# Performance work log

Measured on AMD Instinct MI355X. Metric: run time of the kernel, lower is better.

Reference implementation:

```python
import jax, jax.numpy as jnp
import numpy as np

N_NODES = 100000
N_EDGES = 1600000
N_FEAT = 256
HIDDEN = 128
N_CLASSES = 40


def gcn_conv(x, edge_index, W, b, num_nodes):
    # h = X W  (transform first, like torch_geometric GCNConv)
    h = x @ W  # [N, out]
    # add self loops
    loops = jnp.arange(num_nodes, dtype=edge_index.dtype)
    src = jnp.concatenate([edge_index[0], loops])
    dst = jnp.concatenate([edge_index[1], loops])
    # symmetric normalization: deg computed on dst (in-degree incl. self loop)
    deg = jax.ops.segment_sum(jnp.ones_like(dst, dtype=h.dtype), dst,
                              num_segments=num_nodes)
    dinv = jnp.where(deg > 0, jax.lax.rsqrt(deg), 0.0)
    norm = dinv[src] * dinv[dst]  # [E+N]
    # gather -> scale -> scatter-add
    msgs = h[src] * norm[:, None]
    out = jax.ops.segment_sum(msgs, dst, num_segments=num_nodes)
    return out + b


def setup_inputs() -> dict:
    key = jax.random.key(0)
    k1, k2, k3, k4, k5 = jax.random.split(key, 5)
    x = jax.random.normal(k1, (N_NODES, N_FEAT), dtype=jnp.float32)
    edge_index = jax.random.randint(k2, (2, N_EDGES), 0, N_NODES, dtype=jnp.int64)
    W1 = jax.random.normal(k3, (N_FEAT, HIDDEN), dtype=jnp.float32) * (1.0 / np.sqrt(N_FEAT))
    b1 = jnp.zeros((HIDDEN,), dtype=jnp.float32)
    W2 = jax.random.normal(k4, (HIDDEN, N_CLASSES), dtype=jnp.float32) * (1.0 / np.sqrt(HIDDEN))
    b2 = jnp.zeros((N_CLASSES,), dtype=jnp.float32)
    return {"x": x, "edge_index": edge_index, "W1": W1, "b1": b1, "W2": W2, "b2": b2}


def reference(x, edge_index, W1, b1, W2, b2):
    num_nodes = x.shape[0]
    h = gcn_conv(x, edge_index, W1, b1, num_nodes)
    h = jax.nn.relu(h)
    # dropout p=0.1 is identity in eval mode (self.training == False)
    out = gcn_conv(h, edge_index, W2, b2, num_nodes)
    return out
```

## Files before the change

### kernel.cpp

```cpp
#include <hip/hip_runtime.h>


#define NFEAT 256
#define HID   128
#define NCLS  40
#define NBMAX 3136

__global__ __launch_bounds__(256) void kA_bhist(const int* __restrict__ dst,
                                                int* __restrict__ bcount, int E, int NB) {
    __shared__ int hist[NBMAX];
    for (int i = threadIdx.x; i < NB; i += 256) hist[i] = 0;
    __syncthreads();
    int stride = gridDim.x * blockDim.x;
    for (int e = blockIdx.x * blockDim.x + threadIdx.x; e < E; e += stride)
        atomicAdd(&hist[dst[e] >> 5], 1);
    __syncthreads();
    for (int i = threadIdx.x; i < NB; i += 256) {
        int h = hist[i];
        if (h) atomicAdd(&bcount[i], h);
    }
}

__global__ __launch_bounds__(256) void kB_bscan(const int* __restrict__ bcount,
                                                int* __restrict__ bstart,
                                                int* __restrict__ bcursor,
                                                int* __restrict__ rowptr,
                                                int NB, int Nn, int E) {
    __shared__ int sums[256];
    int t = threadIdx.x;
    int per = (NB + 255) / 256;
    int base = t * per;
    int s = 0;
    for (int j = 0; j < per; j++) {
        int i = base + j;
        if (i < NB) s += bcount[i];
    }
    sums[t] = s;
    __syncthreads();
    for (int off = 1; off < 256; off <<= 1) {
        int v = (t >= off) ? sums[t - off] : 0;
        __syncthreads();
        sums[t] += v;
        __syncthreads();
    }
    int run = sums[t] - s;
    for (int j = 0; j < per; j++) {
        int i = base + j;
        if (i < NB) { bstart[i] = run; bcursor[i] = run; run += bcount[i]; }
    }
    if (t == 255) { bstart[NB] = run; rowptr[Nn] = E; }
}

__global__ __launch_bounds__(256) void kC_scatter(const int* __restrict__ src,
                                                  const int* __restrict__ dst,
                                                  int* __restrict__ bcursor,
                                                  unsigned int* __restrict__ stage, int E) {
    int stride = gridDim.x * blockDim.x;
    for (int e = blockIdx.x * blockDim.x + threadIdx.x; e < E; e += stride) {
        int d = dst[e];
        int pos = atomicAdd(&bcursor[d >> 5], 1);
        stage[pos] = (unsigned int)src[e] | ((unsigned int)(d & 31) << 27);
    }
}

__global__ __launch_bounds__(256) void kD_fill(const unsigned int* __restrict__ stage,
                                               const int* __restrict__ bstart,
                                               int* __restrict__ rowptr,
                                               float* __restrict__ dinv,
                                               int* __restrict__ col, int Nn) {
    __shared__ int deg32[32];
    __shared__ int pref[32];
    __shared__ int cur[32];
    int b = blockIdx.x;
    int t = threadIdx.x;
    int bs = bstart[b], be = bstart[b + 1];
    if (t < 32) deg32[t] = 0;
    __syncthreads();
    for (int i = bs + t; i < be; i += 256) {
        unsigned int u = stage[i];
        atomicAdd(&deg32[u >> 27], 1);
    }
    __syncthreads();
    if (t == 0) {
        int r = 0;
        for (int j = 0; j < 32; j++) { pref[j] = r; r += deg32[j]; }
    }
    __syncthreads();
    int n0 = b * 32;
    if (t < 32) {
        int n = n0 + t;
        if (n < Nn) {
            rowptr[n] = bs + pref[t];
            dinv[n] = rsqrtf((float)(deg32[t] + 1));
        }
        cur[t] = pref[t];
    }
    __syncthreads();
    for (int i = bs + t; i < be; i += 256) {
        unsigned int u = stage[i];
        int d = u >> 27;
        int pos = bs + atomicAdd(&cur[d], 1);
        col[pos] = (int)(u & 0x07FFFFFFu);
    }
}

__global__ __launch_bounds__(256) void k_gemm1(const float* __restrict__ X,
                                               const float* __restrict__ W,
                                               const float* __restrict__ dinv,
                                               float* __restrict__ H, int M) {
    __shared__ float As[32][132];
    __shared__ float Bs[32][128];
    int t = threadIdx.x;
    int tx = t & 15, ty = t >> 4;
    int row0 = blockIdx.x * 128;

    float acc[8][8];
#pragma unroll
    for (int i = 0; i < 8; i++)
#pragma unroll
        for (int j = 0; j < 8; j++) acc[i][j] = 0.f;

    int arow = t >> 3;
    int acol = (t & 7) * 4;
    int brow = t >> 5;
    int bcol = (t & 31) * 4;

    for (int k0 = 0; k0 < NFEAT; k0 += 32) {
#pragma unroll
        for (int p = 0; p < 4; p++) {
            int r = p * 32 + arow;
            int gr = row0 + r;
            float4 v = make_float4(0.f, 0.f, 0.f, 0.f);
            if (gr < M) v = *(const float4*)&X[(size_t)gr * NFEAT + k0 + acol];
            As[acol + 0][r] = v.x; As[acol + 1][r] = v.y;
            As[acol + 2][r] = v.z; As[acol + 3][r] = v.w;
        }
#pragma unroll
        for (int p = 0; p < 4; p++) {
            int kr = p * 8 + brow;
            *(float4*)&Bs[kr][bcol] = *(const float4*)&W[(size_t)(k0 + kr) * HID + bcol];
        }
        __syncthreads();
#pragma unroll
        for (int kk = 0; kk < 32; kk++) {
            float a[8], b[8];
            *(float4*)&a[0] = *(const float4*)&As[kk][ty * 8];
            *(float4*)&a[4] = *(const float4*)&As[kk][ty * 8 + 4];
            *(float4*)&b[0] = *(const float4*)&Bs[kk][tx * 4];
            *(float4*)&b[4] = *(const float4*)&Bs[kk][64 + tx * 4];
#pragma unroll
            for (int i = 0; i < 8; i++)
#pragma unroll
                for (int j = 0; j < 8; j++) acc[i][j] += a[i] * b[j];
        }
        __syncthreads();
    }
#pragma unroll
    for (int i = 0; i < 8; i++) {
        int gr = row0 + ty * 8 + i;
        if (gr < M) {
            float dv = dinv[gr];
            float4 v0 = make_float4(acc[i][0] * dv, acc[i][1] * dv, acc[i][2] * dv, acc[i][3] * dv);
            float4 v1 = make_float4(acc[i][4] * dv, acc[i][5] * dv, acc[i][6] * dv, acc[i][7] * dv);
            *(float4*)&H[(size_t)gr * HID + tx * 4] = v0;
            *(float4*)&H[(size_t)gr * HID + 64 + tx * 4] = v1;
        }
    }
}

__global__ __launch_bounds__(256) void k_agg1(const float* __restrict__ H1,
                                              const int* __restrict__ rowptr,
                                              const int* __restrict__ col,
                                              const float* __restrict__ dinv,
                                              const float* __restrict__ b1,
                                              float* __restrict__ out, int N) {
    int node = blockIdx.x * 4 + (threadIdx.x >> 6);
    if (node >= N) return;
    int lane = threadIdx.x & 63;
    int g = lane >> 5;
    int c = lane & 31;

    float4 acc = make_float4(0.f, 0.f, 0.f, 0.f);
    if (g == 0)
        acc = *(const float4*)&H1[(size_t)node * HID + c * 4];

    int e = rowptr[node], e1 = rowptr[node + 1];
    for (; e + 7 < e1; e += 8) {
        int s0 = col[e + g];
        int s1 = col[e + 2 + g];
        int s2 = col[e + 4 + g];
        int s3 = col[e + 6 + g];
        float4 v0 = *(const float4*)&H1[(size_t)s0 * HID + c * 4];
        float4 v1 = *(const float4*)&H1[(size_t)s1 * HID + c * 4];
        float4 v2 = *(const float4*)&H1[(size_t)s2 * HID + c * 4];
        float4 v3 = *(const float4*)&H1[(size_t)s3 * HID + c * 4];
        acc.x += (v0.x + v1.x) + (v2.x + v3.x);
        acc.y += (v0.y + v1.y) + (v2.y + v3.y);
        acc.z += (v0.z + v1.z) + (v2.z + v3.z);
        acc.w += (v0.w + v1.w) + (v2.w + v3.w);
    }
    for (; e + 1 < e1; e += 2) {
        int s = col[e + g];
        float4 v = *(const float4*)&H1[(size_t)s * HID + c * 4];
        acc.x += v.x; acc.y += v.y; acc.z += v.z; acc.w += v.w;
    }
    if (e < e1 && g == 0) {
        int s = col[e];
        float4 v = *(const float4*)&H1[(size_t)s * HID + c * 4];
        acc.x += v.x; acc.y += v.y; acc.z += v.z; acc.w += v.w;
    }
    acc.x += __shfl_xor(acc.x, 32);
    acc.y += __shfl_xor(acc.y, 32);
    acc.z += __shfl_xor(acc.z, 32);
    acc.w += __shfl_xor(acc.w, 32);

    if (g == 0) {
        float dv = dinv[node];
        float4 bb = *(const float4*)&b1[c * 4];
        float4 r;
        r.x = fmaxf(acc.x * dv + bb.x, 0.f);
        r.y = fmaxf(acc.y * dv + bb.y, 0.f);
        r.z = fmaxf(acc.z * dv + bb.z, 0.f);
        r.w = fmaxf(acc.w * dv + bb.w, 0.f);
        *(float4*)&out[(size_t)node * HID + c * 4] = r;
    }
}

__global__ __launch_bounds__(256) void k_gemm2(const float* __restrict__ A,
                                               const float* __restrict__ W,
                                               const float* __restrict__ dinv,
                                               float* __restrict__ H, int M) {
    __shared__ float As[64][129];
    __shared__ float Ws[HID * NCLS];
    int t = threadIdx.x;
    for (int idx = t; idx < HID * NCLS; idx += 256) Ws[idx] = W[idx];

    int row0 = blockIdx.x * 64;
#pragma unroll
    for (int p = 0; p < 8; p++) {
        int flat = (p * 256 + t) * 4;
        int r = flat >> 7;
        int c = flat & 127;
        int gr = row0 + r;
        float4 v = make_float4(0.f, 0.f, 0.f, 0.f);
        if (gr < M) v = *(const float4*)&A[(size_t)gr * HID + c];
        As[r][c + 0] = v.x; As[r][c + 1] = v.y; As[r][c + 2] = v.z; As[r][c + 3] = v.w;
    }
    __syncthreads();

    int r = t >> 2;
    int cg = (t & 3) * 10;
    float acc[10];
#pragma unroll
    for (int j = 0; j < 10; j++) acc[j] = 0.f;
    for (int k = 0; k < HID; k++) {
        float a = As[r][k];
        const float* wrow = &Ws[k * NCLS + cg];
#pragma unroll
        for (int j = 0; j < 10; j++) acc[j] += a * wrow[j];
    }
    int gr = row0 + r;
    if (gr < M) {
        float dv = dinv[gr];
#pragma unroll
        for (int j = 0; j < 10; j++) H[(size_t)gr * NCLS + cg + j] = acc[j] * dv;
    }
}

__global__ __launch_bounds__(256) void k_agg2(const float* __restrict__ H2,
                                              const int* __restrict__ rowptr,
                                              const int* __restrict__ col,
                                              const float* __restrict__ dinv,
                                              const float* __restrict__ b2,
                                              float* __restrict__ out, int N) {
    int node = blockIdx.x * 4 + (threadIdx.x >> 6);
    if (node >= N) return;
    int lane = threadIdx.x & 63;
    int g = lane / 10;
    int c = lane % 10;
    bool active = g < 6;

    float4 acc = make_float4(0.f, 0.f, 0.f, 0.f);
    if (g == 0)
        acc = *(const float4*)&H2[(size_t)node * NCLS + c * 4];

    int e = rowptr[node], e1 = rowptr[node + 1];
    for (; e + 11 < e1; e += 12) {
        if (active) {
            int s0 = col[e + g];
            int s1 = col[e + 6 + g];
            float4 v0 = *(const float4*)&H2[(size_t)s0 * NCLS + c * 4];
            float4 v1 = *(const float4*)&H2[(size_t)s1 * NCLS + c * 4];
            acc.x += v0.x + v1.x;
            acc.y += v0.y + v1.y;
            acc.z += v0.z + v1.z;
            acc.w += v0.w + v1.w;
        }
    }
    for (; e < e1; e += 6) {
        int idx = e + g;
        if (active && idx < e1) {
            int s = col[idx];
            float4 v = *(const float4*)&H2[(size_t)s * NCLS + c * 4];
            acc.x += v.x; acc.y += v.y; acc.z += v.z; acc.w += v.w;
        }
    }
    float4 t1, t2;
    t1.x = __shfl(acc.x, lane + 30); t1.y = __shfl(acc.y, lane + 30);
    t1.z = __shfl(acc.z, lane + 30); t1.w = __shfl(acc.w, lane + 30);
    acc.x += t1.x; acc.y += t1.y; acc.z += t1.z; acc.w += t1.w;
    t1.x = __shfl(acc.x, lane + 10); t1.y = __shfl(acc.y, lane + 10);
    t1.z = __shfl(acc.z, lane + 10); t1.w = __shfl(acc.w, lane + 10);
    t2.x = __shfl(acc.x, lane + 20); t2.y = __shfl(acc.y, lane + 20);
    t2.z = __shfl(acc.z, lane + 20); t2.w = __shfl(acc.w, lane + 20);
    acc.x += t1.x + t2.x; acc.y += t1.y + t2.y;
    acc.z += t1.z + t2.z; acc.w += t1.w + t2.w;

    if (g == 0) {
        float dv = dinv[node];
        float4 bb = *(const float4*)&b2[c * 4];
        float4 r;
        r.x = acc.x * dv + bb.x;
        r.y = acc.y * dv + bb.y;
        r.z = acc.z * dv + bb.z;
        r.w = acc.w * dv + bb.w;
        *(float4*)&out[(size_t)node * NCLS + c * 4] = r;
    }
}

extern "C" void kernel_launch(void* const* d_in, const int* in_sizes, int n_in,
                              void* d_out, int out_size, void* d_ws, size_t ws_size,
                              hipStream_t stream) {
    const float* x  = (const float*)d_in[0];
    const int*   ei = (const int*)d_in[1];
    const float* W1 = (const float*)d_in[2];
    const float* b1 = (const float*)d_in[3];
    const float* W2 = (const float*)d_in[4];
    const float* b2 = (const float*)d_in[5];
    float* out = (float*)d_out;

    const int N = in_sizes[0] / NFEAT;
    const int E = in_sizes[1] / 2;
    const int NB = (N + 31) / 32;
    const int* src = ei;
    const int* dst = ei + E;

    char* ws = (char*)d_ws;
    size_t off = 0;
    auto alloc = [&](size_t bytes) { size_t cur = off; off = (off + bytes + 255) & ~255ULL; return cur; };
    int*   rowptr  = (int*)(ws + alloc(((size_t)N + 1) * 4));
    float* dinv    = (float*)(ws + alloc((size_t)N * 4));
    int*   bcount  = (int*)(ws + alloc(((size_t)NB + 1) * 4));
    int*   bstart  = (int*)(ws + alloc(((size_t)NB + 1) * 4));
    int*   bcursor = (int*)(ws + alloc(((size_t)NB + 1) * 4));
    int*   colv    = (int*)(ws + alloc((size_t)E * 4));
    float* h1s     = (float*)(ws + alloc((size_t)N * HID * 4));
    float* hrelu   = (float*)(ws + alloc((size_t)N * HID * 4));
    float* h2s     = h1s;
    unsigned int* stage = (unsigned int*)hrelu;

    hipMemsetAsync(bcount, 0, ((size_t)NB + 1) * 4, stream);

    kA_bhist<<<128, 256, 0, stream>>>(dst, bcount, E, NB);
    kB_bscan<<<1, 256, 0, stream>>>(bcount, bstart, bcursor, rowptr, NB, N, E);
    kC_scatter<<<2048, 256, 0, stream>>>(src, dst, bcursor, stage, E);
    kD_fill<<<NB, 256, 0, stream>>>(stage, bstart, rowptr, dinv, colv, N);

    k_gemm1<<<(N + 127) / 128, 256, 0, stream>>>(x, W1, dinv, h1s, N);
    k_agg1<<<(N + 3) / 4, 256, 0, stream>>>(h1s, rowptr, colv, dinv, b1, hrelu, N);
    k_gemm2<<<(N + 63) / 64, 256, 0, stream>>>(hrelu, W2, dinv, h2s, N);
    k_agg2<<<(N + 3) / 4, 256, 0, stream>>>(h2s, rowptr, colv, dinv, b2, out, N);
}
```

Measured before the change: 641.4 us.

## Use 512-node buckets with block-local aggregated atomics for CSR build

Coarse buckets grow from 32 to 512 destination nodes, so there are about 196 buckets instead of about 3125. The scatter pass now builds a per-chunk shared-memory histogram and reserves bucket ranges with one global atomic per bucket per block, replacing one global atomic per edge. The fill kernel uses a 512-entry local histogram with a block scan. Packing the source into 17 bits assumes N ≤ 131072, and NB ≤ 256 caps the node count, so the code is tied to this problem size.

```diff
diff --git a/kernel.cpp b/kernel.cpp
--- a/kernel.cpp
+++ b/kernel.cpp
@@ -4,20 +4,23 @@
 #define NFEAT 256
 #define HID   128
 #define NCLS  40
-#define NBMAX 3136
+#define BSH   9
+#define SRCBITS 17
+#define SRCMASK 0x1FFFF
+#define CHUNK 4096
 
 __global__ __launch_bounds__(256) void kA_bhist(const int* __restrict__ dst,
                                                 int* __restrict__ bcount, int E, int NB) {
-    __shared__ int hist[NBMAX];
-    for (int i = threadIdx.x; i < NB; i += 256) hist[i] = 0;
+    __shared__ int hist[256];
+    if (threadIdx.x < NB) hist[threadIdx.x] = 0;
     __syncthreads();
     int stride = gridDim.x * blockDim.x;
     for (int e = blockIdx.x * blockDim.x + threadIdx.x; e < E; e += stride)
-        atomicAdd(&hist[dst[e] >> 5], 1);
-    __syncthreads();
-    for (int i = threadIdx.x; i < NB; i += 256) {
-        int h = hist[i];
-        if (h) atomicAdd(&bcount[i], h);
+        atomicAdd(&hist[dst[e] >> BSH], 1);
+    __syncthreads();
+    if (threadIdx.x < NB) {
+        int h = hist[threadIdx.x];
+        if (h) atomicAdd(&bcount[threadIdx.x], h);
     }
 }
 
@@ -28,13 +31,7 @@
                                                 int NB, int Nn, int E) {
     __shared__ int sums[256];
     int t = threadIdx.x;
-    int per = (NB + 255) / 256;
-    int base = t * per;
-    int s = 0;
-    for (int j = 0; j < per; j++) {
-        int i = base + j;
-        if (i < NB) s += bcount[i];
-    }
+    int s = (t < NB) ? bcount[t] : 0;
     sums[t] = s;
     __syncthreads();
     for (int off = 1; off < 256; off <<= 1) {
@@ -44,63 +41,91 @@
         __syncthreads();
     }
     int run = sums[t] - s;
-    for (int j = 0; j < per; j++) {
-        int i = base + j;
-        if (i < NB) { bstart[i] = run; bcursor[i] = run; run += bcount[i]; }
-    }
-    if (t == 255) { bstart[NB] = run; rowptr[Nn] = E; }
-}
-
-__global__ __launch_bounds__(256) void kC_scatter(const int* __restrict__ src,
-                                                  const int* __restrict__ dst,
-                                                  int* __restrict__ bcursor,
-                                                  unsigned int* __restrict__ stage, int E) {
-    int stride = gridDim.x * blockDim.x;
-    for (int e = blockIdx.x * blockDim.x + threadIdx.x; e < E; e += stride) {
-        int d = dst[e];
-        int pos = atomicAdd(&bcursor[d >> 5], 1);
-        stage[pos] = (unsigned int)src[e] | ((unsigned int)(d & 31) << 27);
-    }
-}
-
-__global__ __launch_bounds__(256) void kD_fill(const unsigned int* __restrict__ stage,
-                                               const int* __restrict__ bstart,
-                                               int* __restrict__ rowptr,
-                                               float* __restrict__ dinv,
-                                               int* __restrict__ col, int Nn) {
-    __shared__ int deg32[32];
-    __shared__ int pref[32];
-    __shared__ int cur[32];
+    if (t < NB) { bstart[t] = run; bcursor[t] = run; }
+    if (t == 255) { bstart[NB] = sums[255]; rowptr[Nn] = E; }
+}
+
+__global__ __launch_bounds__(256) void kP1(const int* __restrict__ src,
+                                           const int* __restrict__ dst,
+                                           int* __restrict__ bcursor,
+                                           unsigned int* __restrict__ stage,
+                                           int E, int NB) {
+    __shared__ int cnt[256];
+    __shared__ int base[256];
+    int t = threadIdx.x;
+    int e0 = blockIdx.x * CHUNK;
+    if (t < NB) cnt[t] = 0;
+    __syncthreads();
+#pragma unroll
+    for (int j = 0; j < CHUNK / 256; j++) {
+        int e = e0 + j * 256 + t;
+        if (e < E) atomicAdd(&cnt[dst[e] >> BSH], 1);
+    }
+    __syncthreads();
+    if (t < NB) {
+        int c = cnt[t];
+        base[t] = c ? atomicAdd(&bcursor[t], c) : 0;
+        cnt[t] = 0;
+    }
+    __syncthreads();
+#pragma unroll
+    for (int j = 0; j < CHUNK / 256; j++) {
+        int e = e0 + j * 256 + t;
+        if (e < E) {
+            int d = dst[e];
+            int b = d >> BSH;
+            int off = atomicAdd(&cnt[b], 1);
+            stage[base[b] + off] =
+                (unsigned int)src[e] | ((unsigned int)(d & ((1 << BSH) - 1)) << SRCBITS);
+        }
+    }
+}
+
+__global__ __launch_bounds__(256) void kP2(const unsigned int* __restrict__ stage,
+                                           const int* __restrict__ bstart,
+                                           int* __restrict__ rowptr,
+                                           float* __restrict__ dinv,
+                                           int* __restrict__ col, int Nn) {
+    __shared__ int deg[512];
+    __shared__ int cur[512];
+    __shared__ int sums[256];
     int b = blockIdx.x;
     int t = threadIdx.x;
     int bs = bstart[b], be = bstart[b + 1];
-    if (t < 32) deg32[t] = 0;
+    deg[t] = 0; deg[t + 256] = 0;
+    __syncthreads();
+    for (int i = bs + t; i < be; i += 256)
+        atomicAdd(&deg[stage[i] >> SRCBITS], 1);
+    __syncthreads();
+    int d0 = deg[2 * t], d1 = deg[2 * t + 1];
+    int s = d0 + d1;
+    sums[t] = s;
+    __syncthreads();
+    for (int off = 1; off < 256; off <<= 1) {
+        int v = (t >= off) ? sums[t - off] : 0;
+        __syncthreads();
+        sums[t] += v;
+        __syncthreads();
+    }
+    int pref = sums[t] - s;
+    int n0 = b << BSH;
+    int n = n0 + 2 * t;
+    if (n < Nn) {
+        rowptr[n] = bs + pref;
+        dinv[n] = rsqrtf((float)(d0 + 1));
+    }
+    if (n + 1 < Nn) {
+        rowptr[n + 1] = bs + pref + d0;
+        dinv[n + 1] = rsqrtf((float)(d1 + 1));
+    }
+    cur[2 * t] = pref;
+    cur[2 * t + 1] = pref + d0;
     __syncthreads();
     for (int i = bs + t; i < be; i += 256) {
         unsigned int u = stage[i];
-        atomicAdd(&deg32[u >> 27], 1);
-    }
-    __syncthreads();
-    if (t == 0) {
-        int r = 0;
-        for (int j = 0; j < 32; j++) { pref[j] = r; r += deg32[j]; }
-    }
-    __syncthreads();
-    int n0 = b * 32;
-    if (t < 32) {
-        int n = n0 + t;
-        if (n < Nn) {
-            rowptr[n] = bs + pref[t];
-            dinv[n] = rsqrtf((float)(deg32[t] + 1));
-        }
-        cur[t] = pref[t];
-    }
-    __syncthreads();
-    for (int i = bs + t; i < be; i += 256) {
-        unsigned int u = stage[i];
-        int d = u >> 27;
-        int pos = bs + atomicAdd(&cur[d], 1);
-        col[pos] = (int)(u & 0x07FFFFFFu);
+        int dn = u >> SRCBITS;
+        int pos = bs + atomicAdd(&cur[dn], 1);
+        col[pos] = (int)(u & SRCMASK);
     }
 }
 
@@ -341,7 +366,7 @@
 
     const int N = in_sizes[0] / NFEAT;
     const int E = in_sizes[1] / 2;
-    const int NB = (N + 31) / 32;
+    const int NB = (N + (1 << BSH) - 1) >> BSH;
     const int* src = ei;
     const int* dst = ei + E;
 
@@ -363,8 +388,8 @@
 
     kA_bhist<<<128, 256, 0, stream>>>(dst, bcount, E, NB);
     kB_bscan<<<1, 256, 0, stream>>>(bcount, bstart, bcursor, rowptr, NB, N, E);
-    kC_scatter<<<2048, 256, 0, stream>>>(src, dst, bcursor, stage, E);
-    kD_fill<<<NB, 256, 0, stream>>>(stage, bstart, rowptr, dinv, colv, N);
+    kP1<<<(E + CHUNK - 1) / CHUNK, 256, 0, stream>>>(src, dst, bcursor, stage, E, NB);
+    kP2<<<NB, 256, 0, stream>>>(stage, bstart, rowptr, dinv, colv, N);
 
     k_gemm1<<<(N + 127) / 128, 256, 0, stream>>>(x, W1, dinv, h1s, N);
     k_agg1<<<(N + 3) / 4, 256, 0, stream>>>(h1s, rowptr, colv, dinv, b1, hrelu, N);
```

Result: faster. 544.4 us (-15.1%).
